# Kernel optimization log

Hardware: AMD Instinct MI355X
Metric: run time of the kernel (lower is better)

## Reference

```python
import jax, jax.numpy as jnp
import numpy as np

N = 50000
E = 800000
IN_C = 128
OUT_C = 64
NEG_SLOPE = 0.2


def setup_inputs() -> dict:
    key = jax.random.key(0)
    k1, k2, k3, k4, k5 = jax.random.split(key, 5)
    x = jax.random.normal(k1, (N, IN_C), dtype=jnp.float32)
    edge_index = jax.random.randint(k2, (2, E), 0, N, dtype=jnp.int64)
    # GATv2Conv params (heads=1): lin_l (source), lin_r (target), att, bias
    sc_in = 1.0 / np.sqrt(IN_C)
    sc_out = 1.0 / np.sqrt(OUT_C)
    W_l = jax.random.normal(k3, (IN_C, OUT_C), dtype=jnp.float32) * sc_in
    W_r = jax.random.normal(k4, (IN_C, OUT_C), dtype=jnp.float32) * sc_in
    att = jax.random.normal(k5, (OUT_C,), dtype=jnp.float32) * sc_out
    bias = jnp.zeros((OUT_C,), dtype=jnp.float32)
    return {"x": x, "edge_index": edge_index, "W_l": W_l, "W_r": W_r,
            "att": att, "bias": bias}


def _gatv2(x, edge_index, W_l, W_r, att, bias):
    n = x.shape[0]
    # add self loops (PyG default add_self_loops=True)
    loop = jnp.arange(n, dtype=edge_index.dtype)
    src = jnp.concatenate([edge_index[0], loop])
    dst = jnpp_concat = jnp.concatenate([edge_index[1], loop])
    x_l = x @ W_l  # source transform [N, C]
    x_r = x @ W_r  # target transform [N, C]
    x_j = x_l[src]                      # [E+N, C] gathered source msgs
    e = jax.nn.leaky_relu(x_j + x_r[dst], NEG_SLOPE)
    logit = e @ att                     # [E+N]
    # segment softmax over edges grouped by destination node
    m = jax.ops.segment_max(logit, dst, num_segments=n)
    m = jnp.where(jnp.isfinite(m), m, 0.0)
    a = jnp.exp(logit - m[dst])
    denom = jax.ops.segment_sum(a, dst, num_segments=n)
    alpha = a / (denom[dst] + 1e-16)
    out = jax.ops.segment_sum(x_j * alpha[:, None], dst, num_segments=n)
    return out + bias


def reference(x, edge_index, W_l, W_r, att, bias):
    # dropout(p=0.6) is identity at inference
    h = jax.nn.elu(_gatv2(x, edge_index, W_l, W_r, att, bias))
    return jax.nn.log_softmax(h, axis=-1)
```

## Files before the change

### kernel.cpp

```cpp
#include <hip/hip_runtime.h>

#define N_NODES 50000
#define N_EDGES 800000
#define E_TOT   (N_EDGES + N_NODES)
#define IN_C    128
#define OUT_C   64
#define NEG_SLOPE 0.2f

#define CAP     64
#define NPART   6250

#define FILL_CHUNK  1024
#define FILL_NCHUNK ((E_TOT + FILL_CHUNK - 1) / FILL_CHUNK)

#define G_GEMM  ((N_NODES + 63) / 64)
#define G_FILL  (FILL_NCHUNK * 8)

typedef __bf16 bf16_8 __attribute__((ext_vector_type(8)));
typedef float  f32x4  __attribute__((ext_vector_type(4)));

__device__ __forceinline__ unsigned f2bf(float f) {
    unsigned u = __float_as_uint(f);
    return (u + 0x7fffu + ((u >> 16) & 1u)) >> 16;
}

__global__ __launch_bounds__(256) void k_prep(
    const float* __restrict__ Wl, const float* __restrict__ Wr,
    unsigned short* __restrict__ wtg)
{
    int i = blockIdx.x * 256 + threadIdx.x;
    int k = i >> 6, cm = i & 63;
    if (k < 128) {
        wtg[(size_t)cm * 128 + k]        = (unsigned short)f2bf(Wl[(size_t)k * 64 + cm]);
        wtg[(size_t)(64 + cm) * 128 + k] = (unsigned short)f2bf(Wr[(size_t)k * 64 + cm]);
    }
}

#define XPAD 136
__global__ __launch_bounds__(256) void k_gemm_fill(
    const float* __restrict__ x, const unsigned short* __restrict__ wtg,
    const float* __restrict__ att, const int* __restrict__ ei,
    int* __restrict__ cnt, unsigned short* __restrict__ csr_src,
    unsigned short* __restrict__ xlb, float* __restrict__ xr,
    float* __restrict__ qtil)
{
    __shared__ unsigned short xs[64 * XPAD];

    const int tid = threadIdx.x;

    if (blockIdx.x >= G_GEMM) {
        int bid   = blockIdx.x - G_GEMM;
        int part  = bid & 7;
        int chunk = bid >> 3;
        int lo = part * NPART, hi = lo + NPART;
#pragma unroll
        for (int i = 0; i < 4; ++i) {
            int e = chunk * FILL_CHUNK + i * 256 + tid;
            if (e >= E_TOT) break;
            int dst = (e < N_EDGES) ? ei[N_EDGES + e] : e - N_EDGES;
            if (dst >= lo && dst < hi) {
                int src = (e < N_EDGES) ? ei[e] : dst;
                int pos = atomicAdd(&cnt[dst], 1);
                if (pos < CAP) csr_src[(size_t)dst * CAP + pos] = (unsigned short)src;
            }
        }
        return;
    }

    const int nbase = blockIdx.x * 64;

    const float4* x4 = (const float4*)x;
    for (int i = tid; i < 2048; i += 256) {
        int row = i >> 5, qq = i & 31;
        int node = nbase + row;
        float4 v = make_float4(0.f, 0.f, 0.f, 0.f);
        if (node < N_NODES) v = x4[(size_t)node * 32 + qq];
        uint2 p;
        p.x = f2bf(v.x) | (f2bf(v.y) << 16);
        p.y = f2bf(v.z) | (f2bf(v.w) << 16);
        *(uint2*)&xs[row * XPAD + qq * 4] = p;
    }
    __syncthreads();

    const int lane = tid & 63, wave = tid >> 6;
    const int m = lane & 15, quad = lane >> 4;

    bf16_8 af[4];
#pragma unroll
    for (int kt = 0; kt < 4; ++kt)
        af[kt] = *(const bf16_8*)&xs[(wave * 16 + m) * XPAD + kt * 32 + quad * 8];

    f32x4 accs[4];
#pragma unroll
    for (int t = 0; t < 4; ++t) {
        f32x4 acc = {0.f, 0.f, 0.f, 0.f};
#pragma unroll
        for (int kt = 0; kt < 4; ++kt) {
            bf16_8 bfr = *(const bf16_8*)&wtg[(size_t)(t * 16 + m) * 128 + kt * 32 + quad * 8];
            acc = __builtin_amdgcn_mfma_f32_16x16x32_bf16(af[kt], bfr, acc, 0, 0, 0);
        }
        accs[t] = acc;
#pragma unroll
        for (int r = 0; r < 4; ++r) {
            int node = nbase + wave * 16 + quad * 4 + r;
            if (node < N_NODES)
                xlb[(size_t)node * 64 + t * 16 + m] = (unsigned short)f2bf(acc[r]);
        }
    }
    {
        float am[4];
#pragma unroll
        for (int t = 0; t < 4; ++t) am[t] = 0.6f * att[t * 16 + m];
        float part[4];
#pragma unroll
        for (int r = 0; r < 4; ++r) {
            part[r] = am[0] * accs[0][r];
#pragma unroll
            for (int t = 1; t < 4; ++t) part[r] = fmaf(am[t], accs[t][r], part[r]);
        }
#pragma unroll
        for (int o = 1; o <= 8; o <<= 1)
#pragma unroll
            for (int r = 0; r < 4; ++r) part[r] += __shfl_xor(part[r], o);
        if (m == 0) {
#pragma unroll
            for (int r = 0; r < 4; ++r) {
                int node = nbase + wave * 16 + quad * 4 + r;
                if (node < N_NODES) qtil[node] = part[r];
            }
        }
    }
#pragma unroll
    for (int t = 4; t < 8; ++t) {
        f32x4 acc = {0.f, 0.f, 0.f, 0.f};
#pragma unroll
        for (int kt = 0; kt < 4; ++kt) {
            bf16_8 bfr = *(const bf16_8*)&wtg[(size_t)(t * 16 + m) * 128 + kt * 32 + quad * 8];
            acc = __builtin_amdgcn_mfma_f32_16x16x32_bf16(af[kt], bfr, acc, 0, 0, 0);
        }
        int col = t * 16 + m - 64;
#pragma unroll
        for (int r = 0; r < 4; ++r) {
            int node = nbase + wave * 16 + quad * 4 + r;
            if (node < N_NODES) xr[(size_t)node * 64 + col] = acc[r];
        }
    }
}

__global__ __launch_bounds__(256) void k_fused(
    const int* __restrict__ cnt, const unsigned short* __restrict__ csr_src,
    const unsigned short* __restrict__ xlb, const float* __restrict__ xr,
    const float* __restrict__ qtil, const float* __restrict__ att,
    const float* __restrict__ bias, float* __restrict__ out)
{
    int wid  = (blockIdx.x * 256 + threadIdx.x) >> 6;
    if (wid >= N_NODES) return;
    int lane = threadIdx.x & 63;
    int g = lane >> 3;
    int q = lane & 7;

    const uint4* xl4 = (const uint4*)xlb;
    const unsigned short* cs = csr_src + (size_t)wid * CAP;

    const float4* xrp = (const float4*)(xr + (size_t)wid * 64 + q * 8);
    float4 xra = xrp[0], xrb = xrp[1];
    const float4* atp = (const float4*)(att + q * 8);
    float4 ata = atp[0], atb = atp[1];
    float xrv[8] = {xra.x, xra.y, xra.z, xra.w, xrb.x, xrb.y, xrb.z, xrb.w};
    float atv[8] = {ata.x, ata.y, ata.z, ata.w, atb.x, atb.y, atb.z, atb.w};
#pragma unroll
    for (int j = 0; j < 8; ++j) atv[j] *= 0.4f;

    int deg = cnt[wid];
    if (deg > CAP) deg = CAP;
    int iters = (deg + 7) >> 3;

    float s = 0.f;
    float acc[8] = {0.f, 0.f, 0.f, 0.f, 0.f, 0.f, 0.f, 0.f};

    int e = g;
    bool va = e < deg;
    int sA = va ? (int)cs[e] : wid;
    uint4 A = xl4[(size_t)sA * 8 + q];
    float QA = qtil[sA];
    e += 8;
    bool vb = e < deg;
    int sB = vb ? (int)cs[e] : wid;
    uint4 B = xl4[(size_t)sB * 8 + q];
    float QB = qtil[sB];

    for (int it = 0; it < iters; ++it) {
        uint4 C = A; float QC = QA; bool vc = va;
        A = B; QA = QB; va = vb;
        e += 8;
        vb = e < deg;
        int sN = vb ? (int)cs[e] : wid;
        B = xl4[(size_t)sN * 8 + q];
        QB = qtil[sN];

        float c[8];
        c[0] = __uint_as_float(C.x << 16);
        c[1] = __uint_as_float(C.x & 0xffff0000u);
        c[2] = __uint_as_float(C.y << 16);
        c[3] = __uint_as_float(C.y & 0xffff0000u);
        c[4] = __uint_as_float(C.z << 16);
        c[5] = __uint_as_float(C.z & 0xffff0000u);
        c[6] = __uint_as_float(C.w << 16);
        c[7] = __uint_as_float(C.w & 0xffff0000u);

        float r = 0.f;
#pragma unroll
        for (int j = 0; j < 8; ++j) {
            float t = c[j] + xrv[j];
            r = fmaf(atv[j], fabsf(t), r);
        }
        r += __shfl_xor(r, 1);
        r += __shfl_xor(r, 2);
        r += __shfl_xor(r, 4);

        float w = vc ? __expf(QC + r) : 0.f;
        s += w;
#pragma unroll
        for (int j = 0; j < 8; ++j) acc[j] = fmaf(w, c[j], acc[j]);
    }

#pragma unroll
    for (int o = 8; o <= 32; o <<= 1) {
        s += __shfl_xor(s, o);
#pragma unroll
        for (int j = 0; j < 8; ++j) acc[j] += __shfl_xor(acc[j], o);
    }

    float inv = 1.f / (s + 1e-16f);
    const float4* bp = (const float4*)(bias + q * 8);
    float4 ba = bp[0], bb = bp[1];
    float bv[8] = {ba.x, ba.y, ba.z, ba.w, bb.x, bb.y, bb.z, bb.w};
    float h[8];
    float mx = -INFINITY;
#pragma unroll
    for (int j = 0; j < 8; ++j) {
        float hh = fmaf(acc[j], inv, bv[j]);
        hh = (hh > 0.f) ? hh : (__expf(hh) - 1.f);
        h[j] = hh;
        mx = fmaxf(mx, hh);
    }
#pragma unroll
    for (int o = 1; o <= 4; o <<= 1) mx = fmaxf(mx, __shfl_xor(mx, o));
    float ex = 0.f;
#pragma unroll
    for (int j = 0; j < 8; ++j) ex += __expf(h[j] - mx);
#pragma unroll
    for (int o = 1; o <= 4; o <<= 1) ex += __shfl_xor(ex, o);
    float lse = mx + __logf(ex);

    if (g == 0) {
        float4* op = (float4*)(out + (size_t)wid * 64 + q * 8);
        op[0] = make_float4(h[0] - lse, h[1] - lse, h[2] - lse, h[3] - lse);
        op[1] = make_float4(h[4] - lse, h[5] - lse, h[6] - lse, h[7] - lse);
    }
}

extern "C" void kernel_launch(void* const* d_in, const int* in_sizes, int n_in,
                              void* d_out, int out_size, void* d_ws, size_t ws_size,
                              hipStream_t stream)
{
    const float* x    = (const float*)d_in[0];
    const int*   ei   = (const int*)  d_in[1];
    const float* Wl   = (const float*)d_in[2];
    const float* Wr   = (const float*)d_in[3];
    const float* att  = (const float*)d_in[4];
    const float* bias = (const float*)d_in[5];
    float* out = (float*)d_out;

    char* w = (char*)d_ws;
    unsigned short* xlb = (unsigned short*)w; w += (size_t)N_NODES * 64 * 2;
    float* xr      = (float*)w;  w += (size_t)N_NODES * 64 * 4;
    unsigned short* csr_src = (unsigned short*)w; w += (size_t)N_NODES * CAP * 2;
    int*   cnt     = (int*)w;    w += (size_t)N_NODES * 4;
    float* qtil    = (float*)w;  w += (size_t)N_NODES * 4;
    unsigned short* wtg = (unsigned short*)w; w += (size_t)128 * 128 * 2;

    hipMemsetAsync(cnt, 0, (size_t)N_NODES * 4, stream);

    k_prep     <<<32,                         256, 0, stream>>>(Wl, Wr, wtg);
    k_gemm_fill<<<G_GEMM + G_FILL,            256, 0, stream>>>(
        x, wtg, att, ei, cnt, csr_src, xlb, xr, qtil);
    k_fused    <<<(N_NODES * 64 + 255) / 256, 256, 0, stream>>>(
        cnt, csr_src, xlb, xr, qtil, att, bias, out);
}
```

Baseline: 157.2 us.

## Replace 8-pass partitioned CSR fill with bucket pass plus scatter kernel

The edge fill no longer makes every edge chunk read the edge list eight times, once per destination partition. Each chunk now reads its edges once, counts them per partition with shared-memory atomics, reserves space with one global atomic per partition, and writes packed (dst,src) words into per-partition buckets. A new scatter kernel then walks each bucket and does the per-node atomic CSR insert, so atomics on the same node range come from nearby blocks. This adds an extra kernel launch and a bucket round-trip through global memory, and edges beyond the fixed bucket capacity of 120000 would be silently dropped.

```diff
diff --git a/kernel.cpp b/kernel.cpp
--- a/kernel.cpp
+++ b/kernel.cpp
@@ -9,12 +9,12 @@
 
 #define CAP     64
 #define NPART   6250
+#define BKTCAP  120000
 
 #define FILL_CHUNK  1024
-#define FILL_NCHUNK ((E_TOT + FILL_CHUNK - 1) / FILL_CHUNK)
+#define NBKT_A  ((E_TOT + FILL_CHUNK - 1) / FILL_CHUNK)
 
 #define G_GEMM  ((N_NODES + 63) / 64)
-#define G_FILL  (FILL_NCHUNK * 8)
 
 typedef __bf16 bf16_8 __attribute__((ext_vector_type(8)));
 typedef float  f32x4  __attribute__((ext_vector_type(4)));
@@ -37,31 +37,46 @@
 }
 
 #define XPAD 136
-__global__ __launch_bounds__(256) void k_gemm_fill(
+__global__ __launch_bounds__(256) void k_gemm_bucket(
     const float* __restrict__ x, const unsigned short* __restrict__ wtg,
     const float* __restrict__ att, const int* __restrict__ ei,
-    int* __restrict__ cnt, unsigned short* __restrict__ csr_src,
+    int* __restrict__ gcnt, unsigned* __restrict__ bucket,
     unsigned short* __restrict__ xlb, float* __restrict__ xr,
     float* __restrict__ qtil)
 {
     __shared__ unsigned short xs[64 * XPAD];
+    __shared__ int lcnt[8], lbase[8];
 
     const int tid = threadIdx.x;
 
     if (blockIdx.x >= G_GEMM) {
-        int bid   = blockIdx.x - G_GEMM;
-        int part  = bid & 7;
-        int chunk = bid >> 3;
-        int lo = part * NPART, hi = lo + NPART;
+        int bid = blockIdx.x - G_GEMM;
+        if (tid < 8) lcnt[tid] = 0;
+        __syncthreads();
+        int part[4], pos[4]; unsigned pk[4]; bool val[4];
+        int ebase = bid * FILL_CHUNK + tid;
 #pragma unroll
         for (int i = 0; i < 4; ++i) {
-            int e = chunk * FILL_CHUNK + i * 256 + tid;
-            if (e >= E_TOT) break;
-            int dst = (e < N_EDGES) ? ei[N_EDGES + e] : e - N_EDGES;
-            if (dst >= lo && dst < hi) {
-                int src = (e < N_EDGES) ? ei[e] : dst;
-                int pos = atomicAdd(&cnt[dst], 1);
-                if (pos < CAP) csr_src[(size_t)dst * CAP + pos] = (unsigned short)src;
+            int e = ebase + i * 256;
+            val[i] = e < E_TOT;
+            if (val[i]) {
+                int dst, src;
+                if (e < N_EDGES) { src = ei[e]; dst = ei[N_EDGES + e]; }
+                else             { src = dst = e - N_EDGES; }
+                part[i] = dst / NPART;
+                pk[i]   = ((unsigned)dst << 16) | (unsigned)src;
+                pos[i]  = atomicAdd(&lcnt[part[i]], 1);
+            }
+        }
+        __syncthreads();
+        if (tid < 8) lbase[tid] = atomicAdd(&gcnt[tid], lcnt[tid]);
+        __syncthreads();
+#pragma unroll
+        for (int i = 0; i < 4; ++i) {
+            if (val[i]) {
+                int p = part[i];
+                int o = lbase[p] + pos[i];
+                if (o < BKTCAP) bucket[(size_t)p * BKTCAP + o] = pk[i];
             }
         }
         return;
@@ -147,6 +162,23 @@
     }
 }
 
+__global__ __launch_bounds__(256) void k_scatter(
+    const unsigned* __restrict__ bucket, const int* __restrict__ gcnt,
+    int* __restrict__ cnt, unsigned short* __restrict__ csr_src)
+{
+    int part = blockIdx.x & 7;
+    int blk  = blockIdx.x >> 3;
+    int n = gcnt[part];
+    if (n > BKTCAP) n = BKTCAP;
+    const unsigned* b = bucket + (size_t)part * BKTCAP;
+    for (int i = blk * 256 + threadIdx.x; i < n; i += 64 * 256) {
+        unsigned pk = b[i];
+        int dst = pk >> 16, src = pk & 0xffff;
+        int pos = atomicAdd(&cnt[dst], 1);
+        if (pos < CAP) csr_src[(size_t)dst * CAP + pos] = (unsigned short)src;
+    }
+}
+
 __global__ __launch_bounds__(256) void k_fused(
     const int* __restrict__ cnt, const unsigned short* __restrict__ csr_src,
     const unsigned short* __restrict__ xlb, const float* __restrict__ xr,
@@ -277,14 +309,17 @@
     float* xr      = (float*)w;  w += (size_t)N_NODES * 64 * 4;
     unsigned short* csr_src = (unsigned short*)w; w += (size_t)N_NODES * CAP * 2;
     int*   cnt     = (int*)w;    w += (size_t)N_NODES * 4;
+    int*   gcnt    = (int*)w;    w += (size_t)16 * 4;
     float* qtil    = (float*)w;  w += (size_t)N_NODES * 4;
     unsigned short* wtg = (unsigned short*)w; w += (size_t)128 * 128 * 2;
-
-    hipMemsetAsync(cnt, 0, (size_t)N_NODES * 4, stream);
-
-    k_prep     <<<32,                         256, 0, stream>>>(Wl, Wr, wtg);
-    k_gemm_fill<<<G_GEMM + G_FILL,            256, 0, stream>>>(
-        x, wtg, att, ei, cnt, csr_src, xlb, xr, qtil);
-    k_fused    <<<(N_NODES * 64 + 255) / 256, 256, 0, stream>>>(
+    unsigned* bucket = (unsigned*)w; w += (size_t)8 * BKTCAP * 4;
+
+    hipMemsetAsync(cnt, 0, (size_t)(N_NODES + 16) * 4, stream);
+
+    k_prep       <<<32,                         256, 0, stream>>>(Wl, Wr, wtg);
+    k_gemm_bucket<<<G_GEMM + NBKT_A,            256, 0, stream>>>(
+        x, wtg, att, ei, gcnt, bucket, xlb, xr, qtil);
+    k_scatter    <<<512,                        256, 0, stream>>>(bucket, gcnt, cnt, csr_src);
+    k_fused      <<<(N_NODES * 64 + 255) / 256, 256, 0, stream>>>(
         cnt, csr_src, xlb, xr, qtil, att, bias, out);
 }
```

After: 181.1 us. +15.2%, slower.
